# Optimization experiments

Hardware: AMD Instinct MI355X
Metric: run time of the kernel (lower is better)

Reference implementation:

```python
import jax, jax.numpy as jnp
import numpy as np

D, LEN_IN, LEN_OUT = 2, 1, 10
H1, H2 = 32, 32
B, T = 4096, 512
F_IN = D * LEN_IN          # 2
F_OUT = D * LEN_OUT        # 20


def setup_inputs() -> dict:
    key = jax.random.key(0)
    ks = jax.random.split(key, 12)
    s = 1.0 / np.sqrt(H1)  # PyTorch default init scale for LSTMCell/Linear
    u = lambda k, shape: jax.random.uniform(k, shape, jnp.float32, -s, s)
    return {
        "x": jax.random.normal(ks[0], (B, T, F_IN), jnp.float32),
        # LSTMCell 1 (input 2 -> hidden 32); gate order i,f,g,o stacked on dim 0
        "W_ih1": u(ks[1], (4 * H1, F_IN)),
        "W_hh1": u(ks[2], (4 * H1, H1)),
        "b_ih1": u(ks[3], (4 * H1,)),
        "b_hh1": u(ks[4], (4 * H1,)),
        # LSTMCell 2 (32 -> 32)
        "W_ih2": u(ks[5], (4 * H2, H1)),
        "W_hh2": u(ks[6], (4 * H2, H2)),
        "b_ih2": u(ks[7], (4 * H2,)),
        "b_hh2": u(ks[8], (4 * H2,)),
        # Final linear 32 -> 20
        "W_out": u(ks[9], (F_OUT, H2)),
        "b_out": u(ks[10], (F_OUT,)),
    }


def _lstm_cell(x, h, c, W_ih, W_hh, b):
    # gates: [B, 4H]; PyTorch gate order i, f, g, o
    gates = x @ W_ih.T + h @ W_hh.T + b
    i, f, g, o = jnp.split(gates, 4, axis=-1)
    i, f, o = jax.nn.sigmoid(i), jax.nn.sigmoid(f), jax.nn.sigmoid(o)
    g = jnp.tanh(g)
    c_new = f * c + i * g
    h_new = o * jnp.tanh(c_new)
    return h_new, c_new


def reference(x, W_ih1, W_hh1, b_ih1, b_hh1, W_ih2, W_hh2, b_ih2, b_hh2, W_out, b_out):
    b1 = b_ih1 + b_hh1
    b2 = b_ih2 + b_hh2
    Bsz = x.shape[0]
    h1 = jnp.zeros((Bsz, H1), x.dtype)
    c1 = jnp.zeros((Bsz, H1), x.dtype)
    h2 = jnp.zeros((Bsz, H2), x.dtype)
    c2 = jnp.zeros((Bsz, H2), x.dtype)

    def step(carry, x_t):
        h1, c1, h2, c2 = carry
        h1, c1 = _lstm_cell(x_t, h1, c1, W_ih1, W_hh1, b1)
        h2, c2 = _lstm_cell(h1, h2, c2, W_ih2, W_hh2, b2)
        out_t = h2 @ W_out.T + b_out  # [B, 20]
        return (h1, c1, h2, c2), out_t

    xs = jnp.swapaxes(x, 0, 1)  # [T, B, F_IN]
    _, outs = jax.lax.scan(step, (h1, c1, h2, c2), xs)  # outs: [T, B, 20]
    outs = jnp.swapaxes(outs, 0, 1)  # [B, T, 20]
    return outs.reshape(Bsz, x.shape[1], D, LEN_OUT)
```

## Files before the change

kernel.cpp:

```cpp
#include <hip/hip_runtime.h>
#include <hip/hip_fp16.h>

#define TLEN 512
#define HDIM 32
#define FOUT 20
#define HST  36

typedef __attribute__((ext_vector_type(8))) short bf16x8;
typedef __attribute__((ext_vector_type(4))) float f32x4;
typedef __attribute__((ext_vector_type(4))) short s16x4;

__device__ __forceinline__ float sigm(float v) {
  float e = __builtin_amdgcn_exp2f(-1.4426950408889634f * v);
  return __builtin_amdgcn_rcpf(1.0f + e);
}
__device__ __forceinline__ float tanh_f(float v) {
  float e = __builtin_amdgcn_exp2f(2.8853900817779268f * v);
  return 1.0f - 2.0f * __builtin_amdgcn_rcpf(1.0f + e);
}
__device__ __forceinline__ void hilo(float v, short& h, short& l) {
  unsigned u = __builtin_bit_cast(unsigned, v);
  unsigned r = u + 0x7fffu + ((u >> 16) & 1u);
  h = (short)(r >> 16);
  float hf = __builtin_bit_cast(float, r & 0xffff0000u);
  float res = v - hf;
  unsigned u2 = __builtin_bit_cast(unsigned, res);
  unsigned r2 = u2 + 0x7fffu + ((u2 >> 16) & 1u);
  l = (short)(r2 >> 16);
}

__device__ __forceinline__ void barrier_lgkm() {
  asm volatile("s_waitcnt lgkmcnt(0)\n\ts_barrier" ::: "memory");
}

__device__ __forceinline__ bf16x8 read_h(const short* buf, int off) {
  s16x4 a = *(const s16x4*)(buf + off);
  s16x4 b = *(const s16x4*)(buf + off + 4);
  bf16x8 r;
  r[0]=a[0]; r[1]=a[1]; r[2]=a[2]; r[3]=a[3];
  r[4]=b[0]; r[5]=b[1]; r[6]=b[2]; r[7]=b[3];
  return r;
}

__device__ __forceinline__ float lstm_update(const f32x4& g, float& c) {
  float iv = sigm(g[0]), fv = sigm(g[1]), gv = tanh_f(g[2]), ov = sigm(g[3]);
  c = fv * c + iv * gv;
  return ov * tanh_f(c);
}

__global__ __launch_bounds__(512, 2) void lstm_seq_kernel(
    const float* __restrict__ xg,
    const float* __restrict__ Wih1, const float* __restrict__ Whh1,
    const float* __restrict__ bih1, const float* __restrict__ bhh1,
    const float* __restrict__ Wih2, const float* __restrict__ Whh2,
    const float* __restrict__ bih2, const float* __restrict__ bhh2,
    const float* __restrict__ Wout, const float* __restrict__ bout,
    float* __restrict__ out)
{
  __shared__ __half xl[16 * 1028];
  __shared__ short h1hiB[2][16 * HST], h1loB[2][16 * HST];
  __shared__ short h2hiB[2][16 * HST], h2loB[2][16 * HST];

  const int tid  = threadIdx.x;
  const int w    = tid >> 6;
  const int lane = tid & 63;
  const int n    = lane & 15;
  const int q    = lane >> 4;
  const int q4   = q * 4;
  const int q8   = q * 8;
  const int b0   = blockIdx.x * 16;
  const int p    = w & 1;

  for (int idx = tid; idx < 16 * 1024; idx += 512) {
    int row = idx >> 10, col = idx & 1023;
    xl[row * 1028 + col] = __float2half(xg[((size_t)(b0 + row) << 10) + col]);
  }

  const int og = (n & 3) * HDIM + 4 * w + (n >> 2);
  bf16x8 Whh1h, Whh1l, Wih2h, Wih2l, Whh2h, Whh2l;
  #pragma unroll
  for (int j = 0; j < 8; j++) {
    short hh, ll;
    hilo(Whh1[og * HDIM + q8 + j], hh, ll); Whh1h[j] = hh; Whh1l[j] = ll;
    hilo(Wih2[og * HDIM + q8 + j], hh, ll); Wih2h[j] = hh; Wih2l[j] = ll;
    hilo(Whh2[og * HDIM + q8 + j], hh, ll); Whh2h[j] = hh; Whh2l[j] = ll;
  }
  float b1c[4], b2c[4], wx0[4], wx1[4], boc[4];
  #pragma unroll
  for (int r = 0; r < 4; r++) {
    int gr = r * HDIM + 4 * w + q;
    b1c[r] = bih1[gr] + bhh1[gr];
    b2c[r] = bih2[gr] + bhh2[gr];
    wx0[r] = Wih1[gr * 2 + 0];
    wx1[r] = Wih1[gr * 2 + 1];
    int orow = 16 * p + q4 + r;
    boc[r] = (orow < FOUT) ? bout[orow] : 0.0f;
  }
  bf16x8 WoH = {0,0,0,0,0,0,0,0}, WoL = {0,0,0,0,0,0,0,0};
  {
    int orow = 16 * p + n;
    if (orow < FOUT) {
      #pragma unroll
      for (int j = 0; j < 8; j++) {
        short hh, ll;
        hilo(Wout[orow * HDIM + q8 + j], hh, ll); WoH[j] = hh; WoL[j] = ll;
      }
    }
  }

  const int hoff = n * HST + 4 * w + q;
  const int aoff = n * HST + q8;
  float c1 = 0.0f, c2 = 0.0f;

  bf16x8 h1h = {0,0,0,0,0,0,0,0}, h1l = {0,0,0,0,0,0,0,0};
  bf16x8 h2h = {0,0,0,0,0,0,0,0}, h2l = {0,0,0,0,0,0,0,0};

  __syncthreads();

  {
    __half2 hv = *(const __half2*)&xl[n * 1028];
    float xv0 = __half2float(hv.x), xv1 = __half2float(hv.y);
    f32x4 g1;
    #pragma unroll
    for (int r = 0; r < 4; r++) g1[r] = fmaf(xv1, wx1[r], fmaf(xv0, wx0[r], b1c[r]));
    float h1n = lstm_update(g1, c1);
    short hh, ll; hilo(h1n, hh, ll);
    h1hiB[0][hoff] = hh; h1loB[0][hoff] = ll;
    barrier_lgkm();
    h1h = read_h(h1hiB[0], aoff);
    h1l = read_h(h1loB[0], aoff);
  }

  for (int t = 1; t < TLEN; ++t) {
    const int par = t & 1;
    __half2 hv = *(const __half2*)&xl[n * 1028 + 2 * t];
    float xv0 = __half2float(hv.x), xv1 = __half2float(hv.y);

    f32x4 g1;
    #pragma unroll
    for (int r = 0; r < 4; r++) g1[r] = fmaf(xv1, wx1[r], fmaf(xv0, wx0[r], b1c[r]));
    g1 = __builtin_amdgcn_mfma_f32_16x16x32_bf16(Whh1h, h1h, g1, 0, 0, 0);
    g1 = __builtin_amdgcn_mfma_f32_16x16x32_bf16(Whh1l, h1h, g1, 0, 0, 0);
    g1 = __builtin_amdgcn_mfma_f32_16x16x32_bf16(Whh1h, h1l, g1, 0, 0, 0);

    f32x4 ga, gb;
    #pragma unroll
    for (int r = 0; r < 4; r++) { ga[r] = b2c[r]; gb[r] = 0.0f; }
    ga = __builtin_amdgcn_mfma_f32_16x16x32_bf16(Wih2h, h1h, ga, 0, 0, 0);
    gb = __builtin_amdgcn_mfma_f32_16x16x32_bf16(Whh2h, h2h, gb, 0, 0, 0);
    ga = __builtin_amdgcn_mfma_f32_16x16x32_bf16(Wih2l, h1h, ga, 0, 0, 0);
    gb = __builtin_amdgcn_mfma_f32_16x16x32_bf16(Whh2l, h2h, gb, 0, 0, 0);
    ga = __builtin_amdgcn_mfma_f32_16x16x32_bf16(Wih2h, h1l, ga, 0, 0, 0);
    gb = __builtin_amdgcn_mfma_f32_16x16x32_bf16(Whh2h, h2l, gb, 0, 0, 0);

    float h1n = lstm_update(g1, c1);
    f32x4 g2;
    #pragma unroll
    for (int r = 0; r < 4; r++) g2[r] = ga[r] + gb[r];
    float h2n = lstm_update(g2, c2);

    short hh, ll;
    hilo(h1n, hh, ll); h1hiB[par][hoff] = hh; h1loB[par][hoff] = ll;
    hilo(h2n, hh, ll); h2hiB[par][hoff] = hh; h2loB[par][hoff] = ll;

    barrier_lgkm();

    h1h = read_h(h1hiB[par], aoff);
    h1l = read_h(h1loB[par], aoff);
    h2h = read_h(h2hiB[par], aoff);
    h2l = read_h(h2loB[par], aoff);

    const int s = t - 1;
    if ((w >> 1) == (s & 3)) {
      f32x4 ao;
      #pragma unroll
      for (int r = 0; r < 4; r++) ao[r] = boc[r];
      ao = __builtin_amdgcn_mfma_f32_16x16x32_bf16(WoH, h2h, ao, 0, 0, 0);
      ao = __builtin_amdgcn_mfma_f32_16x16x32_bf16(WoL, h2h, ao, 0, 0, 0);
      ao = __builtin_amdgcn_mfma_f32_16x16x32_bf16(WoH, h2l, ao, 0, 0, 0);
      if (p == 0 || q == 0) {
        float4 st = { ao[0], ao[1], ao[2], ao[3] };
        *(float4*)&out[((size_t)(b0 + n) * TLEN + s) * FOUT + 16 * p + q4] = st;
      }
    }
  }

  {
    f32x4 ga, gb;
    #pragma unroll
    for (int r = 0; r < 4; r++) { ga[r] = b2c[r]; gb[r] = 0.0f; }
    ga = __builtin_amdgcn_mfma_f32_16x16x32_bf16(Wih2h, h1h, ga, 0, 0, 0);
    gb = __builtin_amdgcn_mfma_f32_16x16x32_bf16(Whh2h, h2h, gb, 0, 0, 0);
    ga = __builtin_amdgcn_mfma_f32_16x16x32_bf16(Wih2l, h1h, ga, 0, 0, 0);
    gb = __builtin_amdgcn_mfma_f32_16x16x32_bf16(Whh2l, h2h, gb, 0, 0, 0);
    ga = __builtin_amdgcn_mfma_f32_16x16x32_bf16(Wih2h, h1l, ga, 0, 0, 0);
    gb = __builtin_amdgcn_mfma_f32_16x16x32_bf16(Whh2h, h2l, gb, 0, 0, 0);
    f32x4 g2;
    #pragma unroll
    for (int r = 0; r < 4; r++) g2[r] = ga[r] + gb[r];
    float h2n = lstm_update(g2, c2);
    short hh, ll; hilo(h2n, hh, ll);
    h2hiB[0][hoff] = hh; h2loB[0][hoff] = ll;
    barrier_lgkm();
    h2h = read_h(h2hiB[0], aoff);
    h2l = read_h(h2loB[0], aoff);
    const int s = TLEN - 1;
    if ((w >> 1) == (s & 3)) {
      f32x4 ao;
      #pragma unroll
      for (int r = 0; r < 4; r++) ao[r] = boc[r];
      ao = __builtin_amdgcn_mfma_f32_16x16x32_bf16(WoH, h2h, ao, 0, 0, 0);
      ao = __builtin_amdgcn_mfma_f32_16x16x32_bf16(WoL, h2h, ao, 0, 0, 0);
      ao = __builtin_amdgcn_mfma_f32_16x16x32_bf16(WoH, h2l, ao, 0, 0, 0);
      if (p == 0 || q == 0) {
        float4 st = { ao[0], ao[1], ao[2], ao[3] };
        *(float4*)&out[((size_t)(b0 + n) * TLEN + s) * FOUT + 16 * p + q4] = st;
      }
    }
  }
}

extern "C" void kernel_launch(void* const* d_in, const int* in_sizes, int n_in,
                              void* d_out, int out_size, void* d_ws, size_t ws_size,
                              hipStream_t stream) {
  const float* xg   = (const float*)d_in[0];
  const float* Wih1 = (const float*)d_in[1];
  const float* Whh1 = (const float*)d_in[2];
  const float* bih1 = (const float*)d_in[3];
  const float* bhh1 = (const float*)d_in[4];
  const float* Wih2 = (const float*)d_in[5];
  const float* Whh2 = (const float*)d_in[6];
  const float* bih2 = (const float*)d_in[7];
  const float* bhh2 = (const float*)d_in[8];
  const float* Wout = (const float*)d_in[9];
  const float* bout = (const float*)d_in[10];
  float* out = (float*)d_out;

  hipLaunchKernelGGL(lstm_seq_kernel, dim3(256), dim3(512), 0, stream,
                     xg, Wih1, Whh1, bih1, bhh1, Wih2, Whh2, bih2, bhh2, Wout, bout, out);
}
```

Measured before the change: 502.1 us.

## Halve batch per block and split layer-1/layer-2 cell updates across lane halves

Each block now handles 8 batch rows instead of 16 and twice as many blocks are launched. The unused half of the MFMA N dimension computes the layer-2 cell update: lanes n<8 update layer 1 and lanes n>=8 update layer 2 for the same batch rows, with the layer-2 gates moved over by a DPP row xor-8. This halves the transcendental work per lane per step, and the occupancy hint rises to 4 blocks per CU so more independent sequences can hide the serial recurrence latency. The h buffers are merged into one array, x is kept in fp32 in LDS rather than fp16, and the MFMA accumulator chains are split to shorten dependencies. In exchange, half of each MFMA's N columns carry redundant batch columns, and more registers are needed per CU.

```diff
diff --git a/kernel.cpp b/kernel.cpp
--- a/kernel.cpp
+++ b/kernel.cpp
@@ -7,8 +7,8 @@
 #define HST  36
 
 typedef __attribute__((ext_vector_type(8))) short bf16x8;
+typedef __attribute__((ext_vector_type(4))) short s16x4;
 typedef __attribute__((ext_vector_type(4))) float f32x4;
-typedef __attribute__((ext_vector_type(4))) short s16x4;
 
 __device__ __forceinline__ float sigm(float v) {
   float e = __builtin_amdgcn_exp2f(-1.4426950408889634f * v);
@@ -28,11 +28,13 @@
   unsigned r2 = u2 + 0x7fffu + ((u2 >> 16) & 1u);
   l = (short)(r2 >> 16);
 }
-
 __device__ __forceinline__ void barrier_lgkm() {
   asm volatile("s_waitcnt lgkmcnt(0)\n\ts_barrier" ::: "memory");
 }
-
+__device__ __forceinline__ float dpp_xor8(float x) {
+  return __builtin_bit_cast(float,
+      __builtin_amdgcn_mov_dpp(__builtin_bit_cast(int, x), 0x128, 0xF, 0xF, true));
+}
 __device__ __forceinline__ bf16x8 read_h(const short* buf, int off) {
   s16x4 a = *(const s16x4*)(buf + off);
   s16x4 b = *(const s16x4*)(buf + off + 4);
@@ -41,14 +43,13 @@
   r[4]=b[0]; r[5]=b[1]; r[6]=b[2]; r[7]=b[3];
   return r;
 }
-
 __device__ __forceinline__ float lstm_update(const f32x4& g, float& c) {
   float iv = sigm(g[0]), fv = sigm(g[1]), gv = tanh_f(g[2]), ov = sigm(g[3]);
   c = fv * c + iv * gv;
   return ov * tanh_f(c);
 }
 
-__global__ __launch_bounds__(512, 2) void lstm_seq_kernel(
+__global__ __launch_bounds__(512, 4) void lstm_seq_kernel(
     const float* __restrict__ xg,
     const float* __restrict__ Wih1, const float* __restrict__ Whh1,
     const float* __restrict__ bih1, const float* __restrict__ bhh1,
@@ -57,9 +58,8 @@
     const float* __restrict__ Wout, const float* __restrict__ bout,
     float* __restrict__ out)
 {
-  __shared__ __half xl[16 * 1028];
-  __shared__ short h1hiB[2][16 * HST], h1loB[2][16 * HST];
-  __shared__ short h2hiB[2][16 * HST], h2loB[2][16 * HST];
+  __shared__ float xl[8 * 1028];
+  __shared__ short hb[4][2][16 * HST];
 
   const int tid  = threadIdx.x;
   const int w    = tid >> 6;
@@ -68,13 +68,19 @@
   const int q    = lane >> 4;
   const int q4   = q * 4;
   const int q8   = q * 8;
-  const int b0   = blockIdx.x * 16;
+  const int b0   = blockIdx.x * 8;
   const int p    = w & 1;
-
-  for (int idx = tid; idx < 16 * 1024; idx += 512) {
-    int row = idx >> 10, col = idx & 1023;
-    xl[row * 1028 + col] = __float2half(xg[((size_t)(b0 + row) << 10) + col]);
-  }
+  const int u    = 4 * w + q;
+  const bool upd1 = (n < 8);
+  const int xr   = (n & 7) * 1028;
+
+  for (int idx = tid; idx < 2048; idx += 512) {
+    int row = idx >> 8, c4 = idx & 255;
+    *(float4*)&xl[row * 1028 + 4 * c4] =
+        *(const float4*)&xg[((size_t)(b0 + row) << 10) + 4 * c4];
+  }
+  for (int idx = tid; idx < 4 * 2 * 16 * HST; idx += 512)
+    (&hb[0][0][0])[idx] = 0;
 
   const int og = (n & 3) * HDIM + 4 * w + (n >> 2);
   bf16x8 Whh1h, Whh1l, Wih2h, Wih2l, Whh2h, Whh2l;
@@ -85,14 +91,14 @@
     hilo(Wih2[og * HDIM + q8 + j], hh, ll); Wih2h[j] = hh; Wih2l[j] = ll;
     hilo(Whh2[og * HDIM + q8 + j], hh, ll); Whh2h[j] = hh; Whh2l[j] = ll;
   }
-  float b1c[4], b2c[4], wx0[4], wx1[4], boc[4];
+  float b1c[4], b2c[4], wxa[4], wxb[4], boc[4];
   #pragma unroll
   for (int r = 0; r < 4; r++) {
-    int gr = r * HDIM + 4 * w + q;
+    int gr = r * HDIM + u;
     b1c[r] = bih1[gr] + bhh1[gr];
     b2c[r] = bih2[gr] + bhh2[gr];
-    wx0[r] = Wih1[gr * 2 + 0];
-    wx1[r] = Wih1[gr * 2 + 1];
+    wxa[r] = Wih1[gr * 2 + 0];
+    wxb[r] = Wih1[gr * 2 + 1];
     int orow = 16 * p + q4 + r;
     boc[r] = (orow < FOUT) ? bout[orow] : 0.0f;
   }
@@ -108,9 +114,13 @@
     }
   }
 
-  const int hoff = n * HST + 4 * w + q;
+  const int woff = (upd1 ? n : (n - 8)) * HST + u;
+  short* whp[2] = { upd1 ? &hb[0][0][0] : &hb[2][0][0],
+                    upd1 ? &hb[0][1][0] : &hb[2][1][0] };
+  short* wlp[2] = { upd1 ? &hb[1][0][0] : &hb[3][0][0],
+                    upd1 ? &hb[1][1][0] : &hb[3][1][0] };
   const int aoff = n * HST + q8;
-  float c1 = 0.0f, c2 = 0.0f;
+  float c = 0.0f;
 
   bf16x8 h1h = {0,0,0,0,0,0,0,0}, h1l = {0,0,0,0,0,0,0,0};
   bf16x8 h2h = {0,0,0,0,0,0,0,0}, h2l = {0,0,0,0,0,0,0,0};
@@ -118,67 +128,67 @@
   __syncthreads();
 
   {
-    __half2 hv = *(const __half2*)&xl[n * 1028];
-    float xv0 = __half2float(hv.x), xv1 = __half2float(hv.y);
-    f32x4 g1;
-    #pragma unroll
-    for (int r = 0; r < 4; r++) g1[r] = fmaf(xv1, wx1[r], fmaf(xv0, wx0[r], b1c[r]));
-    float h1n = lstm_update(g1, c1);
-    short hh, ll; hilo(h1n, hh, ll);
-    h1hiB[0][hoff] = hh; h1loB[0][hoff] = ll;
+    float2 xv = *(const float2*)&xl[xr];
+    if (upd1) {
+      f32x4 g;
+      #pragma unroll
+      for (int r = 0; r < 4; r++) g[r] = fmaf(xv.y, wxb[r], fmaf(xv.x, wxa[r], b1c[r]));
+      float hn = lstm_update(g, c);
+      short hh, ll; hilo(hn, hh, ll);
+      hb[0][0][n * HST + u] = hh; hb[1][0][n * HST + u] = ll;
+    }
     barrier_lgkm();
-    h1h = read_h(h1hiB[0], aoff);
-    h1l = read_h(h1loB[0], aoff);
+    h1h = read_h(&hb[0][0][0], aoff);
+    h1l = read_h(&hb[1][0][0], aoff);
   }
 
   for (int t = 1; t < TLEN; ++t) {
     const int par = t & 1;
-    __half2 hv = *(const __half2*)&xl[n * 1028 + 2 * t];
-    float xv0 = __half2float(hv.x), xv1 = __half2float(hv.y);
-
-    f32x4 g1;
+    float2 xv = *(const float2*)&xl[xr + 2 * t];
+
+    f32x4 g1a, g1b = { 0.0f, 0.0f, 0.0f, 0.0f };
     #pragma unroll
-    for (int r = 0; r < 4; r++) g1[r] = fmaf(xv1, wx1[r], fmaf(xv0, wx0[r], b1c[r]));
-    g1 = __builtin_amdgcn_mfma_f32_16x16x32_bf16(Whh1h, h1h, g1, 0, 0, 0);
-    g1 = __builtin_amdgcn_mfma_f32_16x16x32_bf16(Whh1l, h1h, g1, 0, 0, 0);
-    g1 = __builtin_amdgcn_mfma_f32_16x16x32_bf16(Whh1h, h1l, g1, 0, 0, 0);
-
-    f32x4 ga, gb;
-    #pragma unroll
-    for (int r = 0; r < 4; r++) { ga[r] = b2c[r]; gb[r] = 0.0f; }
+    for (int r = 0; r < 4; r++) g1a[r] = fmaf(xv.y, wxb[r], fmaf(xv.x, wxa[r], b1c[r]));
+    g1a = __builtin_amdgcn_mfma_f32_16x16x32_bf16(Whh1h, h1h, g1a, 0, 0, 0);
+    g1b = __builtin_amdgcn_mfma_f32_16x16x32_bf16(Whh1l, h1h, g1b, 0, 0, 0);
+    g1a = __builtin_amdgcn_mfma_f32_16x16x32_bf16(Whh1h, h1l, g1a, 0, 0, 0);
+
+    f32x4 ga = { b2c[0], b2c[1], b2c[2], b2c[3] };
+    f32x4 gb = { 0.0f, 0.0f, 0.0f, 0.0f };
+    f32x4 gc = { 0.0f, 0.0f, 0.0f, 0.0f };
     ga = __builtin_amdgcn_mfma_f32_16x16x32_bf16(Wih2h, h1h, ga, 0, 0, 0);
     gb = __builtin_amdgcn_mfma_f32_16x16x32_bf16(Whh2h, h2h, gb, 0, 0, 0);
-    ga = __builtin_amdgcn_mfma_f32_16x16x32_bf16(Wih2l, h1h, ga, 0, 0, 0);
-    gb = __builtin_amdgcn_mfma_f32_16x16x32_bf16(Whh2l, h2h, gb, 0, 0, 0);
+    gc = __builtin_amdgcn_mfma_f32_16x16x32_bf16(Wih2l, h1h, gc, 0, 0, 0);
     ga = __builtin_amdgcn_mfma_f32_16x16x32_bf16(Wih2h, h1l, ga, 0, 0, 0);
     gb = __builtin_amdgcn_mfma_f32_16x16x32_bf16(Whh2h, h2l, gb, 0, 0, 0);
-
-    float h1n = lstm_update(g1, c1);
-    f32x4 g2;
+    gc = __builtin_amdgcn_mfma_f32_16x16x32_bf16(Whh2l, h2h, gc, 0, 0, 0);
+
+    f32x4 g;
     #pragma unroll
-    for (int r = 0; r < 4; r++) g2[r] = ga[r] + gb[r];
-    float h2n = lstm_update(g2, c2);
-
-    short hh, ll;
-    hilo(h1n, hh, ll); h1hiB[par][hoff] = hh; h1loB[par][hoff] = ll;
-    hilo(h2n, hh, ll); h2hiB[par][hoff] = hh; h2loB[par][hoff] = ll;
+    for (int r = 0; r < 4; r++) {
+      float g1r = g1a[r] + g1b[r];
+      float g2r = ga[r] + gb[r] + gc[r];
+      float grr = dpp_xor8(g2r);
+      g[r] = upd1 ? g1r : grr;
+    }
+    float hn = lstm_update(g, c);
+    short hh, ll; hilo(hn, hh, ll);
+    whp[par][woff] = hh; wlp[par][woff] = ll;
 
     barrier_lgkm();
 
-    h1h = read_h(h1hiB[par], aoff);
-    h1l = read_h(h1loB[par], aoff);
-    h2h = read_h(h2hiB[par], aoff);
-    h2l = read_h(h2loB[par], aoff);
+    h1h = read_h(&hb[0][par][0], aoff);
+    h1l = read_h(&hb[1][par][0], aoff);
+    h2h = read_h(&hb[2][par][0], aoff);
+    h2l = read_h(&hb[3][par][0], aoff);
 
     const int s = t - 1;
     if ((w >> 1) == (s & 3)) {
-      f32x4 ao;
-      #pragma unroll
-      for (int r = 0; r < 4; r++) ao[r] = boc[r];
+      f32x4 ao = { boc[0], boc[1], boc[2], boc[3] };
       ao = __builtin_amdgcn_mfma_f32_16x16x32_bf16(WoH, h2h, ao, 0, 0, 0);
       ao = __builtin_amdgcn_mfma_f32_16x16x32_bf16(WoL, h2h, ao, 0, 0, 0);
       ao = __builtin_amdgcn_mfma_f32_16x16x32_bf16(WoH, h2l, ao, 0, 0, 0);
-      if (p == 0 || q == 0) {
+      if ((p == 0 || q == 0) && n < 8) {
         float4 st = { ao[0], ao[1], ao[2], ao[3] };
         *(float4*)&out[((size_t)(b0 + n) * TLEN + s) * FOUT + 16 * p + q4] = st;
       }
@@ -186,35 +196,34 @@
   }
 
   {
-    f32x4 ga, gb;
-    #pragma unroll
-    for (int r = 0; r < 4; r++) { ga[r] = b2c[r]; gb[r] = 0.0f; }
+    f32x4 ga = { b2c[0], b2c[1], b2c[2], b2c[3] };
+    f32x4 gb = { 0.0f, 0.0f, 0.0f, 0.0f };
+    f32x4 gc = { 0.0f, 0.0f, 0.0f, 0.0f };
     ga = __builtin_amdgcn_mfma_f32_16x16x32_bf16(Wih2h, h1h, ga, 0, 0, 0);
     gb = __builtin_amdgcn_mfma_f32_16x16x32_bf16(Whh2h, h2h, gb, 0, 0, 0);
-    ga = __builtin_amdgcn_mfma_f32_16x16x32_bf16(Wih2l, h1h, ga, 0, 0, 0);
-    gb = __builtin_amdgcn_mfma_f32_16x16x32_bf16(Whh2l, h2h, gb, 0, 0, 0);
+    gc = __builtin_amdgcn_mfma_f32_16x16x32_bf16(Wih2l, h1h, gc, 0, 0, 0);
     ga = __builtin_amdgcn_mfma_f32_16x16x32_bf16(Wih2h, h1l, ga, 0, 0, 0);
     gb = __builtin_amdgcn_mfma_f32_16x16x32_bf16(Whh2h, h2l, gb, 0, 0, 0);
-    f32x4 g2;
+    gc = __builtin_amdgcn_mfma_f32_16x16x32_bf16(Whh2l, h2h, gc, 0, 0, 0);
+    f32x4 g;
     #pragma unroll
-    for (int r = 0; r < 4; r++) g2[r] = ga[r] + gb[r];
-    float h2n = lstm_update(g2, c2);
-    short hh, ll; hilo(h2n, hh, ll);
-    h2hiB[0][hoff] = hh; h2loB[0][hoff] = ll;
+    for (int r = 0; r < 4; r++) g[r] = dpp_xor8(ga[r] + gb[r] + gc[r]);
+    if (!upd1) {
+      float hn = lstm_update(g, c);
+      short hh, ll; hilo(hn, hh, ll);
+      hb[2][0][(n - 8) * HST + u] = hh; hb[3][0][(n - 8) * HST + u] = ll;
+    }
     barrier_lgkm();
-    h2h = read_h(h2hiB[0], aoff);
-    h2l = read_h(h2loB[0], aoff);
-    const int s = TLEN - 1;
-    if ((w >> 1) == (s & 3)) {
-      f32x4 ao;
-      #pragma unroll
-      for (int r = 0; r < 4; r++) ao[r] = boc[r];
+    h2h = read_h(&hb[2][0][0], aoff);
+    h2l = read_h(&hb[3][0][0], aoff);
+    if ((w >> 1) == 3) {
+      f32x4 ao = { boc[0], boc[1], boc[2], boc[3] };
       ao = __builtin_amdgcn_mfma_f32_16x16x32_bf16(WoH, h2h, ao, 0, 0, 0);
       ao = __builtin_amdgcn_mfma_f32_16x16x32_bf16(WoL, h2h, ao, 0, 0, 0);
       ao = __builtin_amdgcn_mfma_f32_16x16x32_bf16(WoH, h2l, ao, 0, 0, 0);
-      if (p == 0 || q == 0) {
+      if ((p == 0 || q == 0) && n < 8) {
         float4 st = { ao[0], ao[1], ao[2], ao[3] };
-        *(float4*)&out[((size_t)(b0 + n) * TLEN + s) * FOUT + 16 * p + q4] = st;
+        *(float4*)&out[((size_t)(b0 + n) * TLEN + 511) * FOUT + 16 * p + q4] = st;
       }
     }
   }
@@ -236,6 +245,6 @@
   const float* bout = (const float*)d_in[10];
   float* out = (float*)d_out;
 
-  hipLaunchKernelGGL(lstm_seq_kernel, dim3(256), dim3(512), 0, stream,
+  hipLaunchKernelGGL(lstm_seq_kernel, dim3(512), dim3(512), 0, stream,
                      xg, Wih1, Whh1, bih1, bhh1, Wih2, Whh2, bih2, bhh2, Wout, bout, out);
 }
```

After: 635.5 us. +26.6%, slower.
